# Optimization experiments

Measured on AMD Instinct MI355X. Metric: run time of the kernel, lower is better.

Reference implementation:

```python
import jax, jax.numpy as jnp
import numpy as np

EPS = 1e-5
SLOPE = 0.01  # torch LeakyReLU default


def _bn(h, gamma, beta):
    # BatchNorm1d in training mode: biased batch stats over dim 0
    m = jnp.mean(h, axis=0)
    v = jnp.var(h, axis=0)
    return (h - m) * jax.lax.rsqrt(v + EPS) * gamma + beta


def _leaky(h):
    return jnp.where(h >= 0, h, SLOPE * h)


def _xavier(key, fan_in, fan_out):
    lim = np.sqrt(6.0 / (fan_in + fan_out))
    return jax.random.uniform(key, (fan_in, fan_out), jnp.float32, -lim, lim)


def setup_inputs() -> dict:
    key = jax.random.key(0)
    ks = jax.random.split(key, 12)
    N, E, B = 50000, 800000, 500
    D_NODE, D_EDGE, HID, OUT = 64, 64, 128, 128
    x = jax.random.normal(ks[0], (N, D_NODE), jnp.float32)
    edge_index = jax.random.randint(ks[1], (2, E), 0, N, jnp.int64)
    edge_attr = jax.random.normal(ks[2], (E, D_EDGE), jnp.float32)
    u = jnp.zeros((B, 1), jnp.float32)
    batch = jnp.sort(jax.random.randint(ks[3], (N,), 0, B, jnp.int64))
    b = lambda n: jnp.full((n,), 0.01, jnp.float32)
    return {
        "x": x, "edge_index": edge_index, "edge_attr": edge_attr, "u": u, "batch": batch,
        # global_mlp_1: Lin(128,128) LeakyReLU BN Lin(128,128)
        "W1a": _xavier(ks[4], D_NODE + D_EDGE, HID), "b1a": b(HID),
        "g1a": jnp.ones((HID,), jnp.float32), "be1a": jnp.zeros((HID,), jnp.float32),
        "W2a": _xavier(ks[5], HID, HID), "b2a": b(HID),
        # global_mlp_2: Lin(192,128) LReLU BN Lin(128,128) LReLU BN Lin(128,128)
        "W1b": _xavier(ks[6], HID + D_NODE, HID), "b1b": b(HID),
        "g1b": jnp.ones((HID,), jnp.float32), "be1b": jnp.zeros((HID,), jnp.float32),
        "W2b": _xavier(ks[7], HID, HID), "b2b": b(HID),
        "g2b": jnp.ones((HID,), jnp.float32), "be2b": jnp.zeros((HID,), jnp.float32),
        "W3b": _xavier(ks[8], HID, OUT), "b3b": b(OUT),
    }


def reference(x, edge_index, edge_attr, u, batch,
              W1a, b1a, g1a, be1a, W2a, b2a,
              W1b, b1b, g1b, be1b, W2b, b2b, g2b, be2b, W3b, b3b):
    N = x.shape[0]
    B = u.shape[0]
    row, col = edge_index[0], edge_index[1]
    # gather source nodes, concat edge features -> edge MLP
    h = jnp.concatenate([x[row], edge_attr], axis=1)          # [E, 128]
    h = _bn(_leaky(h @ W1a + b1a), g1a, be1a) @ W2a + b2a     # [E, hid]
    # scatter_add edges -> destination nodes
    node_agg = jax.ops.segment_sum(h, col, num_segments=N)    # [N, hid]
    # per-graph sums
    gx = jax.ops.segment_sum(x, batch, num_segments=B)        # [B, 64]
    ga = jax.ops.segment_sum(node_agg, batch, num_segments=B) # [B, hid]
    g = jnp.concatenate([gx, ga], axis=1)                     # [B, 192]
    g = _bn(_leaky(g @ W1b + b1b), g1b, be1b)
    g = _bn(_leaky(g @ W2b + b2b), g2b, be2b)
    return g @ W3b + b3b                                      # [B, 128]
```

## Files before the change

### kernel.cpp

```cpp
#include <hip/hip_runtime.h>

#define EPS 1e-5f
#define SLOPE 0.01f
#define NBMAX 512

typedef __attribute__((ext_vector_type(8))) short bf16x8;
typedef __attribute__((ext_vector_type(4))) float f32x4;
typedef __attribute__((ext_vector_type(4))) short s16x4;

__device__ __forceinline__ float leaky(float z) { return z >= 0.f ? z : SLOPE * z; }

__device__ __forceinline__ short f2bf(float f) {
    unsigned u = __float_as_uint(f);
    u += 0x7fff + ((u >> 16) & 1);
    return (short)(u >> 16);
}

__device__ __forceinline__ unsigned pack2(float f0, float f1) {
    unsigned u0 = __float_as_uint(f0) + 0x8000u;
    unsigned u1 = __float_as_uint(f1) + 0x8000u;
    return __builtin_amdgcn_perm(u1, u0, 0x07060302u);
}
__device__ __forceinline__ bf16x8 pack8(f32x4 lo, f32x4 hi) {
    union { bf16x8 v; unsigned u[4]; } r;
    r.u[0] = pack2(lo[0], lo[1]);
    r.u[1] = pack2(lo[2], lo[3]);
    r.u[2] = pack2(hi[0], hi[1]);
    r.u[3] = pack2(hi[2], hi[3]);
    return r.v;
}

__global__ __launch_bounds__(256) void k_prep(
    const float* __restrict__ x, short* __restrict__ xb,
    const float* __restrict__ W1a, short* __restrict__ WT,
    const int* __restrict__ ei, const int* __restrict__ batch,
    int* __restrict__ gdst, int* __restrict__ counts, int* __restrict__ node_off,
    int N, int E, int B, int nbx, int nbh, int nbn) {
    __shared__ int h[NBMAX];
    const int bid = blockIdx.x, t = threadIdx.x;
    if (bid < nbx) {
        int i = bid * 256 + t;
        if (i < N * 16) {
            f32x4 v = ((const f32x4*)x)[i];
            s16x4 o;
#pragma unroll
            for (int j = 0; j < 4; ++j) o[j] = f2bf(v[j]);
            ((s16x4*)xb)[i] = o;
        }
    } else if (bid < nbx + nbh) {
        for (int b = t; b < NBMAX; b += 256) h[b] = 0;
        __syncthreads();
        int base = (bid - nbx) * 4096;
#pragma unroll
        for (int i = 0; i < 16; ++i) {
            int e = base + i * 256 + t;
            if (e < E) {
                int g = batch[ei[E + e]];
                gdst[e] = g;
                atomicAdd(&h[g], 1);
            }
        }
        __syncthreads();
        for (int b = t; b < NBMAX; b += 256)
            if (h[b]) atomicAdd(&counts[b], h[b]);
    } else if (bid < nbx + nbh + nbn) {
        int n = (bid - nbx - nbh) * 256 + t;
        if (n < N) {
            int b1 = batch[n];
            int prev = (n == 0) ? -1 : batch[n - 1];
            for (int g = prev + 1; g <= b1; ++g) node_off[g] = n;
            if (n == N - 1)
                for (int g = b1 + 1; g <= B; ++g) node_off[g] = N;
        }
    } else {
        int c = t >> 1, k0 = (t & 1) * 64;
        for (int k = 0; k < 64; ++k)
            WT[c * 128 + k0 + k] = f2bf(W1a[(k0 + k) * 128 + c]);
    }
}

__global__ void k_scan(const int* __restrict__ counts, int* __restrict__ edge_off,
                       int* __restrict__ cursor, int B) {
    __shared__ int s[1024];
    int t = threadIdx.x;
    s[t] = (t < B) ? counts[t] : 0;
    __syncthreads();
    for (int d = 1; d < 1024; d <<= 1) {
        int v = (t >= d) ? s[t - d] : 0;
        __syncthreads();
        s[t] += v;
        __syncthreads();
    }
    if (t <= B) {
        int excl = (t == 0) ? 0 : s[t - 1];
        edge_off[t] = excl;
        if (t < B) cursor[t] = excl;
    }
}

__global__ __launch_bounds__(256) void k_pos(
    const int* __restrict__ gdst, const int* __restrict__ ei,
    int* __restrict__ cursor, int* __restrict__ perm, int* __restrict__ rows_s,
    const float* __restrict__ x, const int* __restrict__ node_off,
    float* __restrict__ gx, int E, int nbh) {
    __shared__ int cnt[NBMAX];
    __shared__ int basep[NBMAX];
    __shared__ float part[4][64];
    const int bid = blockIdx.x, t = threadIdx.x;
    if (bid < nbh) {
        for (int b = t; b < NBMAX; b += 256) cnt[b] = 0;
        __syncthreads();
        int blk = bid * 4096;
        int g[16], rk[16];
#pragma unroll
        for (int i = 0; i < 16; ++i) {
            int e = blk + i * 256 + t;
            g[i] = (e < E) ? gdst[e] : -1;
            rk[i] = (g[i] >= 0) ? atomicAdd(&cnt[g[i]], 1) : 0;
        }
        __syncthreads();
        for (int b = t; b < NBMAX; b += 256) {
            int c = cnt[b];
            basep[b] = c ? atomicAdd(&cursor[b], c) : 0;
        }
        __syncthreads();
#pragma unroll
        for (int i = 0; i < 16; ++i) {
            int e = blk + i * 256 + t;
            if (g[i] >= 0) {
                int pos = basep[g[i]] + rk[i];
                perm[pos] = e;
                rows_s[pos] = ei[e];
            }
        }
    } else {
        int g = bid - nbh;
        int lane = t & 63, wave = t >> 6;
        int n0 = node_off[g], n1 = node_off[g + 1];
        float a = 0.f;
        for (int n = n0 + wave; n < n1; n += 4) a += x[(size_t)n * 64 + lane];
        part[wave][lane] = a;
        __syncthreads();
        if (wave == 0)
            gx[g * 64 + lane] =
                (part[0][lane] + part[1][lane]) + (part[2][lane] + part[3][lane]);
    }
}

__global__ __launch_bounds__(256) void k_edges2(
    const short* __restrict__ xb, const float* __restrict__ ea,
    const int* __restrict__ rows_s, const int* __restrict__ perm,
    const int* __restrict__ edge_off, const short* __restrict__ WT,
    const float* __restrict__ b1a, float* __restrict__ Sg, float* __restrict__ Qg,
    int CH) {
    const int g = blockIdx.x;
    const int lane = threadIdx.x & 63, wave = threadIdx.x >> 6;
    const int m = lane & 15, quad = lane >> 4;

    bf16x8 Wf[4][8];
#pragma unroll
    for (int t = 0; t < 8; ++t)
#pragma unroll
        for (int ks = 0; ks < 4; ++ks)
            Wf[ks][t] = *(const bf16x8*)(WT + (t * 16 + m) * 128 + ks * 32 + quad * 8);
    float bb[8];
#pragma unroll
    for (int t = 0; t < 8; ++t) bb[t] = b1a[t * 16 + m];

    const int e0 = edge_off[g], e1 = edge_off[g + 1];
    const int cnt = e1 - e0;
    const int chunk = (cnt + CH - 1) / CH;
    const int lo = e0 + blockIdx.y * chunk;
    const int hi = min(lo + chunk, e1);

    float accS[8] = {0, 0, 0, 0, 0, 0, 0, 0};
    float accQ[8] = {0, 0, 0, 0, 0, 0, 0, 0};

    for (int ib = lo + wave * 16; ib < hi; ib += 64) {
        int idx = min(ib + m, hi - 1);
        int rid = rows_s[idx];
        int e = perm[idx];
        const short* xr = xb + (size_t)rid * 64;
        bf16x8 A0 = *(const bf16x8*)(xr + quad * 8);
        bf16x8 A1 = *(const bf16x8*)(xr + 32 + quad * 8);
        const float* er = ea + (size_t)e * 64;
        f32x4 p0 = *(const f32x4*)(er + quad * 8);
        f32x4 p1 = *(const f32x4*)(er + quad * 8 + 4);
        f32x4 p2 = *(const f32x4*)(er + 32 + quad * 8);
        f32x4 p3 = *(const f32x4*)(er + 32 + quad * 8 + 4);
        bf16x8 A2 = pack8(p0, p1);
        bf16x8 A3 = pack8(p2, p3);
        if (ib + 16 <= hi) {
#pragma unroll
            for (int t = 0; t < 8; ++t) {
                f32x4 c = {0.f, 0.f, 0.f, 0.f};
                c = __builtin_amdgcn_mfma_f32_16x16x32_bf16(A0, Wf[0][t], c, 0, 0, 0);
                c = __builtin_amdgcn_mfma_f32_16x16x32_bf16(A1, Wf[1][t], c, 0, 0, 0);
                c = __builtin_amdgcn_mfma_f32_16x16x32_bf16(A2, Wf[2][t], c, 0, 0, 0);
                c = __builtin_amdgcn_mfma_f32_16x16x32_bf16(A3, Wf[3][t], c, 0, 0, 0);
#pragma unroll
                for (int r2 = 0; r2 < 4; ++r2) {
                    float z = c[r2] + bb[t];
                    float a = fmaf(SLOPE, fminf(z, 0.f), fmaxf(z, 0.f));
                    accS[t] += a;
                    accQ[t] = fmaf(a, a, accQ[t]);
                }
            }
        } else {
            float vf[4];
#pragma unroll
            for (int r2 = 0; r2 < 4; ++r2)
                vf[r2] = ((ib + quad * 4 + r2) < hi) ? 1.f : 0.f;
#pragma unroll
            for (int t = 0; t < 8; ++t) {
                f32x4 c = {0.f, 0.f, 0.f, 0.f};
                c = __builtin_amdgcn_mfma_f32_16x16x32_bf16(A0, Wf[0][t], c, 0, 0, 0);
                c = __builtin_amdgcn_mfma_f32_16x16x32_bf16(A1, Wf[1][t], c, 0, 0, 0);
                c = __builtin_amdgcn_mfma_f32_16x16x32_bf16(A2, Wf[2][t], c, 0, 0, 0);
                c = __builtin_amdgcn_mfma_f32_16x16x32_bf16(A3, Wf[3][t], c, 0, 0, 0);
#pragma unroll
                for (int r2 = 0; r2 < 4; ++r2) {
                    float z = c[r2] + bb[t];
                    float a = fmaf(SLOPE, fminf(z, 0.f), fmaxf(z, 0.f)) * vf[r2];
                    accS[t] += a;
                    accQ[t] = fmaf(a, a, accQ[t]);
                }
            }
        }
    }
#pragma unroll
    for (int t = 0; t < 8; ++t) {
        float s = accS[t];
        s += __shfl_xor(s, 16);
        s += __shfl_xor(s, 32);
        float q = accQ[t];
        q += __shfl_xor(q, 16);
        q += __shfl_xor(q, 32);
        if (quad == 0) {
            atomicAdd(&Sg[g * 128 + t * 16 + m], s);
            atomicAdd(&Qg[g * 128 + t * 16 + m], q);
        }
    }
}

__global__ __launch_bounds__(128) void k_stats_part(const float* __restrict__ Sg,
                                                    const float* __restrict__ Qg,
                                                    float* __restrict__ Stot,
                                                    float* __restrict__ Qtot, int B) {
    int c = threadIdx.x;
    int per = (B + gridDim.x - 1) / gridDim.x;
    int g0 = blockIdx.x * per, g1 = min(g0 + per, B);
    float S = 0.f, Q = 0.f;
    for (int g = g0; g < g1; ++g) {
        S += Sg[g * 128 + c];
        Q += Qg[g * 128 + c];
    }
    atomicAdd(&Stot[c], S);
    atomicAdd(&Qtot[c], Q);
}

__global__ __launch_bounds__(128) void k_g1(
    const float* __restrict__ Sg, const float* __restrict__ Stot,
    const float* __restrict__ Qtot, const float* __restrict__ gx,
    const int* __restrict__ edge_off, const float* __restrict__ g1a,
    const float* __restrict__ be1a, const float* __restrict__ W2a,
    const float* __restrict__ b2a, const float* __restrict__ W1b,
    const float* __restrict__ b1b, float* __restrict__ a1,
    float* __restrict__ sum1, float* __restrict__ sumsq1, float invE) {
    __shared__ float T[128];
    __shared__ float gcat[192];
    int g = blockIdx.x, c = threadIdx.x;
    float mn = Stot[c] * invE;
    float v = Qtot[c] * invE - mn * mn;
    float sc = g1a[c] * rsqrtf(v + EPS);
    float sh = be1a[c] - mn * sc;
    float cg = (float)(edge_off[g + 1] - edge_off[g]);
    T[c] = Sg[g * 128 + c] * sc + cg * sh;
    if (c < 64) gcat[c] = gx[g * 64 + c];
    __syncthreads();
    float ga = cg * b2a[c];
#pragma unroll 8
    for (int k = 0; k < 128; ++k) ga = fmaf(T[k], W2a[k * 128 + c], ga);
    gcat[64 + c] = ga;
    __syncthreads();
    float z = b1b[c];
#pragma unroll 8
    for (int k = 0; k < 192; ++k) z = fmaf(gcat[k], W1b[k * 128 + c], z);
    float av = leaky(z);
    a1[g * 128 + c] = av;
    atomicAdd(&sum1[c], av);
    atomicAdd(&sumsq1[c], av * av);
}

__global__ __launch_bounds__(128) void k_bn_lin(
    const float* __restrict__ a_prev, const float* __restrict__ sum,
    const float* __restrict__ sumsq, const float* __restrict__ gma,
    const float* __restrict__ bta, const float* __restrict__ W,
    const float* __restrict__ b, float* __restrict__ a_out,
    float* __restrict__ sum_out, float* __restrict__ sumsq_out, float invB,
    int do_leaky) {
    __shared__ float hs[128];
    int g = blockIdx.x, c = threadIdx.x;
    float mn = sum[c] * invB;
    float v = sumsq[c] * invB - mn * mn;
    float sc = gma[c] * rsqrtf(v + EPS);
    float sh = bta[c] - mn * sc;
    hs[c] = a_prev[g * 128 + c] * sc + sh;
    __syncthreads();
    float z = b[c];
#pragma unroll 8
    for (int k = 0; k < 128; ++k) z = fmaf(hs[k], W[k * 128 + c], z);
    if (do_leaky) {
        z = leaky(z);
        a_out[g * 128 + c] = z;
        atomicAdd(&sum_out[c], z);
        atomicAdd(&sumsq_out[c], z * z);
    } else {
        a_out[g * 128 + c] = z;
    }
}

extern "C" void kernel_launch(void* const* d_in, const int* in_sizes, int n_in,
                              void* d_out, int out_size, void* d_ws, size_t ws_size,
                              hipStream_t stream) {
    const float* x    = (const float*)d_in[0];
    const int*   ei   = (const int*)d_in[1];
    const float* ea   = (const float*)d_in[2];
    const int*   batch= (const int*)d_in[4];
    const float* W1a  = (const float*)d_in[5];
    const float* b1a  = (const float*)d_in[6];
    const float* g1a  = (const float*)d_in[7];
    const float* be1a = (const float*)d_in[8];
    const float* W2a  = (const float*)d_in[9];
    const float* b2a  = (const float*)d_in[10];
    const float* W1b  = (const float*)d_in[11];
    const float* b1b  = (const float*)d_in[12];
    const float* g1b  = (const float*)d_in[13];
    const float* be1b = (const float*)d_in[14];
    const float* W2b  = (const float*)d_in[15];
    const float* b2b  = (const float*)d_in[16];
    const float* g2b  = (const float*)d_in[17];
    const float* be2b = (const float*)d_in[18];
    const float* W3b  = (const float*)d_in[19];
    const float* b3b  = (const float*)d_in[20];

    const int N = in_sizes[0] / 64;
    const int E = in_sizes[1] / 2;
    const int B = in_sizes[3];

    char* ws = (char*)d_ws;
    size_t off = 0;
    auto alloc = [&](size_t bytes) -> char* {
        char* p = ws + off;
        off = (off + bytes + 255) & ~(size_t)255;
        return p;
    };
    int*   counts = (int*)alloc((size_t)B * 4);
    float* Sg     = (float*)alloc((size_t)B * 128 * 4);
    float* Qg     = (float*)alloc((size_t)B * 128 * 4);
    float* sum1   = (float*)alloc(128 * 4);
    float* sumsq1 = (float*)alloc(128 * 4);
    float* sum2   = (float*)alloc(128 * 4);
    float* sumsq2 = (float*)alloc(128 * 4);
    float* Stot   = (float*)alloc(128 * 4);
    float* Qtot   = (float*)alloc(128 * 4);
    size_t zbytes = off;
    short* xb      = (short*)alloc((size_t)N * 64 * 2);
    short* WT      = (short*)alloc(128 * 128 * 2);
    int*   gdst    = (int*)alloc((size_t)E * 4);
    int*   perm    = (int*)alloc((size_t)E * 4);
    int*   rows_s  = (int*)alloc((size_t)E * 4);
    int*   edge_off= (int*)alloc((size_t)(B + 1) * 4);
    int*   cursor  = (int*)alloc((size_t)B * 4);
    int*   node_off= (int*)alloc((size_t)(B + 1) * 4);
    float* gx      = (float*)alloc((size_t)B * 64 * 4);
    float* a1      = (float*)alloc((size_t)B * 128 * 4);
    float* a2      = (float*)alloc((size_t)B * 128 * 4);
    (void)ws_size;
    (void)n_in;

    hipMemsetAsync(ws, 0, zbytes, stream);

    const int nbx = (N * 16 + 255) / 256;
    const int nbh = (E + 4095) / 4096;
    const int nbn = (N + 255) / 256;
    k_prep<<<dim3(nbx + nbh + nbn + 1), dim3(256), 0, stream>>>(
        x, xb, W1a, WT, ei, batch, gdst, counts, node_off, N, E, B, nbx, nbh, nbn);
    k_scan<<<dim3(1), dim3(1024), 0, stream>>>(counts, edge_off, cursor, B);
    k_pos<<<dim3(nbh + B), dim3(256), 0, stream>>>(gdst, ei, cursor, perm, rows_s,
                                                   x, node_off, gx, E, nbh);
    const int CH = 2;
    k_edges2<<<dim3(B, CH), dim3(256), 0, stream>>>(xb, ea, rows_s, perm, edge_off,
                                                    WT, b1a, Sg, Qg, CH);
    k_stats_part<<<dim3(25), dim3(128), 0, stream>>>(Sg, Qg, Stot, Qtot, B);
    k_g1<<<dim3(B), dim3(128), 0, stream>>>(Sg, Stot, Qtot, gx, edge_off, g1a, be1a,
                                            W2a, b2a, W1b, b1b, a1, sum1, sumsq1,
                                            1.0f / (float)E);
    k_bn_lin<<<dim3(B), dim3(128), 0, stream>>>(a1, sum1, sumsq1, g1b, be1b, W2b,
                                                b2b, a2, sum2, sumsq2,
                                                1.0f / (float)B, 1);
    k_bn_lin<<<dim3(B), dim3(128), 0, stream>>>(a2, sum2, sumsq2, g2b, be2b, W3b,
                                                b3b, (float*)d_out, nullptr, nullptr,
                                                1.0f / (float)B, 0);
}
```

Before: 481.7 us.

## Software-pipeline edge gathers in k_edges2 and use one 512-thread block per graph

The edge kernel now prefetches the next tile's gathered node rows and edge features into registers while the MFMAs run on the current tile, with index loads fetched two tiles ahead. The goal is to hide gather latency on the memory-bound edge pass. The launch also moves from two 256-thread blocks per graph to a single 512-thread block per graph, which drops the split along the y dimension. The prefetch registers raise VGPR pressure under the 512-thread launch bound, and that can lower occupancy or cause spills.

```diff
diff --git a/kernel.cpp b/kernel.cpp
--- a/kernel.cpp
+++ b/kernel.cpp
@@ -147,12 +147,11 @@
     }
 }
 
-__global__ __launch_bounds__(256) void k_edges2(
+__global__ __launch_bounds__(512) void k_edges2(
     const short* __restrict__ xb, const float* __restrict__ ea,
     const int* __restrict__ rows_s, const int* __restrict__ perm,
     const int* __restrict__ edge_off, const short* __restrict__ WT,
-    const float* __restrict__ b1a, float* __restrict__ Sg, float* __restrict__ Qg,
-    int CH) {
+    const float* __restrict__ b1a, float* __restrict__ Sg, float* __restrict__ Qg) {
     const int g = blockIdx.x;
     const int lane = threadIdx.x & 63, wave = threadIdx.x >> 6;
     const int m = lane & 15, quad = lane >> 4;
@@ -167,78 +166,96 @@
 #pragma unroll
     for (int t = 0; t < 8; ++t) bb[t] = b1a[t * 16 + m];
 
-    const int e0 = edge_off[g], e1 = edge_off[g + 1];
-    const int cnt = e1 - e0;
-    const int chunk = (cnt + CH - 1) / CH;
-    const int lo = e0 + blockIdx.y * chunk;
-    const int hi = min(lo + chunk, e1);
+    const int lo = edge_off[g], hi = edge_off[g + 1];
 
     float accS[8] = {0, 0, 0, 0, 0, 0, 0, 0};
     float accQ[8] = {0, 0, 0, 0, 0, 0, 0, 0};
 
-    for (int ib = lo + wave * 16; ib < hi; ib += 64) {
-        int idx = min(ib + m, hi - 1);
-        int rid = rows_s[idx];
-        int e = perm[idx];
-        const short* xr = xb + (size_t)rid * 64;
-        bf16x8 A0 = *(const bf16x8*)(xr + quad * 8);
-        bf16x8 A1 = *(const bf16x8*)(xr + 32 + quad * 8);
-        const float* er = ea + (size_t)e * 64;
-        f32x4 p0 = *(const f32x4*)(er + quad * 8);
-        f32x4 p1 = *(const f32x4*)(er + quad * 8 + 4);
-        f32x4 p2 = *(const f32x4*)(er + 32 + quad * 8);
-        f32x4 p3 = *(const f32x4*)(er + 32 + quad * 8 + 4);
-        bf16x8 A2 = pack8(p0, p1);
-        bf16x8 A3 = pack8(p2, p3);
-        if (ib + 16 <= hi) {
-#pragma unroll
-            for (int t = 0; t < 8; ++t) {
-                f32x4 c = {0.f, 0.f, 0.f, 0.f};
-                c = __builtin_amdgcn_mfma_f32_16x16x32_bf16(A0, Wf[0][t], c, 0, 0, 0);
-                c = __builtin_amdgcn_mfma_f32_16x16x32_bf16(A1, Wf[1][t], c, 0, 0, 0);
-                c = __builtin_amdgcn_mfma_f32_16x16x32_bf16(A2, Wf[2][t], c, 0, 0, 0);
-                c = __builtin_amdgcn_mfma_f32_16x16x32_bf16(A3, Wf[3][t], c, 0, 0, 0);
-#pragma unroll
-                for (int r2 = 0; r2 < 4; ++r2) {
-                    float z = c[r2] + bb[t];
-                    float a = fmaf(SLOPE, fminf(z, 0.f), fmaxf(z, 0.f));
-                    accS[t] += a;
-                    accQ[t] = fmaf(a, a, accQ[t]);
+    int b = lo + wave * 16;
+    const bool active = (b < hi);
+    if (active) {
+        int i0 = min(b + m, hi - 1);
+        int r0 = rows_s[i0], p0 = perm[i0];
+        int i1 = min(b + 128 + m, hi - 1);
+        int r1 = rows_s[i1], p1 = perm[i1];
+        const short* xr0 = xb + (size_t)r0 * 64;
+        bf16x8 X0 = *(const bf16x8*)(xr0 + quad * 8);
+        bf16x8 X1 = *(const bf16x8*)(xr0 + 32 + quad * 8);
+        const float* er0 = ea + (size_t)p0 * 64;
+        f32x4 P0 = *(const f32x4*)(er0 + quad * 8);
+        f32x4 P1 = *(const f32x4*)(er0 + quad * 8 + 4);
+        f32x4 P2 = *(const f32x4*)(er0 + 32 + quad * 8);
+        f32x4 P3 = *(const f32x4*)(er0 + 32 + quad * 8 + 4);
+
+        while (b < hi) {
+            const int bn = b + 128;
+            int i2 = min(bn + 128 + m, hi - 1);
+            int r2 = rows_s[i2], p2 = perm[i2];
+            const short* xrn = xb + (size_t)r1 * 64;
+            bf16x8 Xn0 = *(const bf16x8*)(xrn + quad * 8);
+            bf16x8 Xn1 = *(const bf16x8*)(xrn + 32 + quad * 8);
+            const float* ern = ea + (size_t)p1 * 64;
+            f32x4 Q0 = *(const f32x4*)(ern + quad * 8);
+            f32x4 Q1 = *(const f32x4*)(ern + quad * 8 + 4);
+            f32x4 Q2 = *(const f32x4*)(ern + 32 + quad * 8);
+            f32x4 Q3 = *(const f32x4*)(ern + 32 + quad * 8 + 4);
+
+            bf16x8 A2 = pack8(P0, P1);
+            bf16x8 A3 = pack8(P2, P3);
+            if (b + 16 <= hi) {
+#pragma unroll
+                for (int t = 0; t < 8; ++t) {
+                    f32x4 c = {0.f, 0.f, 0.f, 0.f};
+                    c = __builtin_amdgcn_mfma_f32_16x16x32_bf16(A2, Wf[2][t], c, 0, 0, 0);
+                    c = __builtin_amdgcn_mfma_f32_16x16x32_bf16(A3, Wf[3][t], c, 0, 0, 0);
+                    c = __builtin_amdgcn_mfma_f32_16x16x32_bf16(X0, Wf[0][t], c, 0, 0, 0);
+                    c = __builtin_amdgcn_mfma_f32_16x16x32_bf16(X1, Wf[1][t], c, 0, 0, 0);
+#pragma unroll
+                    for (int r = 0; r < 4; ++r) {
+                        float z = c[r] + bb[t];
+                        float a = fmaf(SLOPE, fminf(z, 0.f), fmaxf(z, 0.f));
+                        accS[t] += a;
+                        accQ[t] = fmaf(a, a, accQ[t]);
+                    }
+                }
+            } else {
+                float vf[4];
+#pragma unroll
+                for (int r = 0; r < 4; ++r)
+                    vf[r] = ((b + quad * 4 + r) < hi) ? 1.f : 0.f;
+#pragma unroll
+                for (int t = 0; t < 8; ++t) {
+                    f32x4 c = {0.f, 0.f, 0.f, 0.f};
+                    c = __builtin_amdgcn_mfma_f32_16x16x32_bf16(A2, Wf[2][t], c, 0, 0, 0);
+                    c = __builtin_amdgcn_mfma_f32_16x16x32_bf16(A3, Wf[3][t], c, 0, 0, 0);
+                    c = __builtin_amdgcn_mfma_f32_16x16x32_bf16(X0, Wf[0][t], c, 0, 0, 0);
+                    c = __builtin_amdgcn_mfma_f32_16x16x32_bf16(X1, Wf[1][t], c, 0, 0, 0);
+#pragma unroll
+                    for (int r = 0; r < 4; ++r) {
+                        float z = c[r] + bb[t];
+                        float a = fmaf(SLOPE, fminf(z, 0.f), fmaxf(z, 0.f)) * vf[r];
+                        accS[t] += a;
+                        accQ[t] = fmaf(a, a, accQ[t]);
+                    }
                 }
             }
-        } else {
-            float vf[4];
-#pragma unroll
-            for (int r2 = 0; r2 < 4; ++r2)
-                vf[r2] = ((ib + quad * 4 + r2) < hi) ? 1.f : 0.f;
-#pragma unroll
-            for (int t = 0; t < 8; ++t) {
-                f32x4 c = {0.f, 0.f, 0.f, 0.f};
-                c = __builtin_amdgcn_mfma_f32_16x16x32_bf16(A0, Wf[0][t], c, 0, 0, 0);
-                c = __builtin_amdgcn_mfma_f32_16x16x32_bf16(A1, Wf[1][t], c, 0, 0, 0);
-                c = __builtin_amdgcn_mfma_f32_16x16x32_bf16(A2, Wf[2][t], c, 0, 0, 0);
-                c = __builtin_amdgcn_mfma_f32_16x16x32_bf16(A3, Wf[3][t], c, 0, 0, 0);
-#pragma unroll
-                for (int r2 = 0; r2 < 4; ++r2) {
-                    float z = c[r2] + bb[t];
-                    float a = fmaf(SLOPE, fminf(z, 0.f), fmaxf(z, 0.f)) * vf[r2];
-                    accS[t] += a;
-                    accQ[t] = fmaf(a, a, accQ[t]);
-                }
+            X0 = Xn0; X1 = Xn1;
+            P0 = Q0; P1 = Q1; P2 = Q2; P3 = Q3;
+            r1 = r2; p1 = p2;
+            b = bn;
+        }
+#pragma unroll
+        for (int t = 0; t < 8; ++t) {
+            float s = accS[t];
+            s += __shfl_xor(s, 16);
+            s += __shfl_xor(s, 32);
+            float q = accQ[t];
+            q += __shfl_xor(q, 16);
+            q += __shfl_xor(q, 32);
+            if (quad == 0) {
+                atomicAdd(&Sg[g * 128 + t * 16 + m], s);
+                atomicAdd(&Qg[g * 128 + t * 16 + m], q);
             }
-        }
-    }
-#pragma unroll
-    for (int t = 0; t < 8; ++t) {
-        float s = accS[t];
-        s += __shfl_xor(s, 16);
-        s += __shfl_xor(s, 32);
-        float q = accQ[t];
-        q += __shfl_xor(q, 16);
-        q += __shfl_xor(q, 32);
-        if (quad == 0) {
-            atomicAdd(&Sg[g * 128 + t * 16 + m], s);
-            atomicAdd(&Qg[g * 128 + t * 16 + m], q);
         }
     }
 }
@@ -389,9 +406,8 @@
     k_scan<<<dim3(1), dim3(1024), 0, stream>>>(counts, edge_off, cursor, B);
     k_pos<<<dim3(nbh + B), dim3(256), 0, stream>>>(gdst, ei, cursor, perm, rows_s,
                                                    x, node_off, gx, E, nbh);
-    const int CH = 2;
-    k_edges2<<<dim3(B, CH), dim3(256), 0, stream>>>(xb, ea, rows_s, perm, edge_off,
-                                                    WT, b1a, Sg, Qg, CH);
+    k_edges2<<<dim3(B), dim3(512), 0, stream>>>(xb, ea, rows_s, perm, edge_off,
+                                                WT, b1a, Sg, Qg);
     k_stats_part<<<dim3(25), dim3(128), 0, stream>>>(Sg, Qg, Stot, Qtot, B);
     k_g1<<<dim3(B), dim3(128), 0, stream>>>(Sg, Stot, Qtot, gx, edge_off, g1a, be1a,
                                             W2a, b2a, W1b, b1b, a1, sum1, sumsq1,
```

Result: faster. 470.2 us (-2.4%).
